# Optimization experiments

Hardware: AMD Instinct MI355X
Metric: run time of the kernel (lower is better)

Reference implementation:

```python
import jax, jax.numpy as jnp
import numpy as np

EPS_BN = 1e-5


def _square_distance(a, b):
    # a: [B,N,3], b: [B,S,3] -> [B,N,S]
    return (jnp.sum(a * a, -1)[:, :, None]
            - 2.0 * jnp.einsum('bnc,bsc->bns', a, b)
            + jnp.sum(b * b, -1)[:, None, :])


def _bn_relu(x, gamma, beta):
    # x: [B,C,N]; training-mode batch norm over (B,N) per channel
    mean = jnp.mean(x, axis=(0, 2), keepdims=True)
    var = jnp.var(x, axis=(0, 2), keepdims=True)
    y = (x - mean) * jax.lax.rsqrt(var + EPS_BN)
    y = y * gamma[None, :, None] + beta[None, :, None]
    return jax.nn.relu(y)


def setup_inputs() -> dict:
    key = jax.random.key(0)
    ks = jax.random.split(key, 8)
    B, N, S, D1, D2 = 16, 4096, 1024, 128, 256
    Cin, C0, C1 = D1 + D2, 256, 128
    inp = {
        'xyz1': jax.random.normal(ks[0], (B, 3, N), jnp.float32),
        'xyz2': jax.random.normal(ks[1], (B, 3, S), jnp.float32),
        'points1': jax.random.normal(ks[2], (B, D1, N), jnp.float32),
        'points2': jax.random.normal(ks[3], (B, D2, S), jnp.float32),
        # pointwise Conv1d weights (kernel size 1) as [out,in]
        'w0': jax.random.normal(ks[4], (C0, Cin), jnp.float32) * (1.0 / np.sqrt(Cin)),
        'b0': jnp.zeros((C0,), jnp.float32),
        'g0': jnp.ones((C0,), jnp.float32),
        'be0': jnp.zeros((C0,), jnp.float32),
        'w1': jax.random.normal(ks[5], (C1, C0), jnp.float32) * (1.0 / np.sqrt(C0)),
        'b1': jnp.zeros((C1,), jnp.float32),
        'g1': jnp.ones((C1,), jnp.float32),
        'be1': jnp.zeros((C1,), jnp.float32),
    }
    return inp


def reference(xyz1, xyz2, points1, points2, w0, b0, g0, be0, w1, b1, g1, be1):
    # permute to [B,N,3] / [B,S,3] / [B,S,D2]
    x1 = jnp.transpose(xyz1, (0, 2, 1))
    x2 = jnp.transpose(xyz2, (0, 2, 1))
    p2 = jnp.transpose(points2, (0, 2, 1))
    B, N, _ = x1.shape

    dists = _square_distance(x1, x2)            # [B,N,S]
    # NOTE: faithful to the source: idx comes from the sort, but the
    # weight distances are the FIRST 3 columns of the UNsorted dists
    # (the repo assigns sorted values to `dicts`, not `dists`).
    idx = jnp.argsort(dists, axis=-1)[:, :, :3]  # [B,N,3]
    d3 = jnp.maximum(dists[:, :, :3], 1e-10)     # [B,N,3]
    weight = 1.0 / d3
    weight = weight / jnp.sum(weight, axis=-1, keepdims=True)

    gathered = jax.vmap(lambda p, i: p[i])(p2, idx)          # [B,N,3,D2]
    interpolated = jnp.sum(gathered * weight[..., None], axis=2)  # [B,N,D2]

    p1 = jnp.transpose(points1, (0, 2, 1))       # [B,N,D1]
    new_points = jnp.concatenate([p1, interpolated], axis=-1)  # [B,N,Cin]
    new_points = jnp.transpose(new_points, (0, 2, 1))           # [B,Cin,N]

    h = jnp.einsum('oc,bcn->bon', w0, new_points) + b0[None, :, None]
    h = _bn_relu(h, g0, be0)
    h = jnp.einsum('oc,bcn->bon', w1, h) + b1[None, :, None]
    h = _bn_relu(h, g1, be1)
    return h
```

## Files before the change

### kernel.cpp

```cpp
#include <hip/hip_runtime.h>
#include <cstdint>
#include <cstddef>

#define BB   16
#define NN   4096
#define SS   1024
#define D1   128
#define D2   256
#define CIN  384
#define C0   256
#define C1   128
#define MM   (BB*NN)
#define NBLK (MM/128)

typedef __attribute__((ext_vector_type(8))) short short8;
typedef __attribute__((ext_vector_type(4))) float f32x4;

__device__ __forceinline__ float b2f(unsigned short h) {
    union { unsigned int u; float f; } x; x.u = ((unsigned int)h) << 16; return x.f;
}
__device__ __forceinline__ unsigned short f2b(float f) {
    union { float f; unsigned int u; } x; x.f = f;
    unsigned int r = x.u + 0x7FFFu + ((x.u >> 16) & 1u);
    return (unsigned short)(r >> 16);
}

#define GLD16(g, l) __builtin_amdgcn_global_load_lds( \
    (const __attribute__((address_space(1))) void*)(g), \
    (__attribute__((address_space(3))) void*)(l), 16, 0, 0)

__device__ __forceinline__ void knn_body5(const float* __restrict__ xyz1,
                                          const float* __restrict__ xyz2,
                                          int* __restrict__ idxb, float* __restrict__ wtb,
                                          int rb, int t, char* smem)
{
    float4* cnd = (float4*)smem;
    const int b    = rb >> 7;
    const int bx   = rb & 127;
    const int chunk = t & 7;
    const int n    = bx * 32 + (t >> 3);

    for (int i = t; i < SS; i += 256) {
        float qx = xyz2[((size_t)b * 3 + 0) * SS + i];
        float qy = xyz2[((size_t)b * 3 + 1) * SS + i];
        float qz = xyz2[((size_t)b * 3 + 2) * SS + i];
        cnd[(i >> 7) * 129 + (i & 127)] = make_float4(qx, qy, qz, 0.f);
    }
    __syncthreads();

    const float px = xyz1[((size_t)b * 3 + 0) * NN + n];
    const float py = xyz1[((size_t)b * 3 + 1) * NN + n];
    const float pz = xyz1[((size_t)b * 3 + 2) * NN + n];

    const double INITK = __hiloint2double(0x7F7FFFFF, 0);
    double A0 = INITK, A1 = INITK, A2 = INITK;
    double B0 = INITK, B1 = INITK, B2 = INITK;
    const float4* cc = cnd + chunk * 129;
    const int sbase = chunk * 128;

#pragma unroll 4
    for (int c = 0; c < 128; c += 2) {
        {
            float4 q = cc[c];
            float dx = px - q.x, dy = py - q.y, dz = pz - q.z;
            float d = dx*dx + dy*dy + dz*dz;
            double k = __hiloint2double(__float_as_int(d), sbase + c);
            double t0 = fmin(k, A0), h0 = fmax(k, A0);
            double t1 = fmin(h0, A1), h1 = fmax(h0, A1);
            A2 = fmin(h1, A2); A0 = t0; A1 = t1;
        }
        {
            float4 q = cc[c + 1];
            float dx = px - q.x, dy = py - q.y, dz = pz - q.z;
            float d = dx*dx + dy*dy + dz*dz;
            double k = __hiloint2double(__float_as_int(d), sbase + c + 1);
            double t0 = fmin(k, B0), h0 = fmax(k, B0);
            double t1 = fmin(h0, B1), h1 = fmax(h0, B1);
            B2 = fmin(h1, B2); B0 = t0; B1 = t1;
        }
    }

    double K0, K1, K2;
    {
        double y0 = fmax(A0, B0);
        K0 = fmin(A0, B0);
        double x1 = fmin(A1, B1);
        K1 = fmin(y0, x1);
        double z  = fmax(y0, x1);
        K2 = fmin(z, fmin(A2, B2));
    }
#pragma unroll
    for (int r = 1; r <= 4; r <<= 1) {
        double C0d = __shfl_xor(K0, r);
        double C1d = __shfl_xor(K1, r);
        double C2d = __shfl_xor(K2, r);
        double y0 = fmax(K0, C0d);
        K0 = fmin(K0, C0d);
        double x1 = fmin(K1, C1d);
        double nK1 = fmin(y0, x1);
        double z  = fmax(y0, x1);
        K2 = fmin(z, fmin(K2, C2d));
        K1 = nK1;
    }

    if (chunk == 0) {
        int j0 = __double2loint(K0), j1 = __double2loint(K1), j2 = __double2loint(K2);
        float4 q0 = cnd[0], q1 = cnd[1], q2 = cnd[2];
        float dd0, dd1, dd2;
        { float dx=px-q0.x, dy=py-q0.y, dz=pz-q0.z; dd0 = fmaxf(dx*dx+dy*dy+dz*dz, 1e-10f); }
        { float dx=px-q1.x, dy=py-q1.y, dz=pz-q1.z; dd1 = fmaxf(dx*dx+dy*dy+dz*dz, 1e-10f); }
        { float dx=px-q2.x, dy=py-q2.y, dz=pz-q2.z; dd2 = fmaxf(dx*dx+dy*dy+dz*dz, 1e-10f); }
        float r0 = 1.f/dd0, r1 = 1.f/dd1, r2 = 1.f/dd2;
        float inv = 1.f / (r0 + r1 + r2);
        size_t base = ((size_t)b * NN + n) * 3;
        idxb[base+0] = j0; idxb[base+1] = j1; idxb[base+2] = j2;
        wtb[base+0] = r0*inv; wtb[base+1] = r1*inv; wtb[base+2] = r2*inv;
    }
}

__device__ __forceinline__ void transpose_body(const float* __restrict__ src,
                                               unsigned short* __restrict__ dst,
                                               int C, int Np, int dstStride,
                                               int b, int cblk, int nblk, int t, char* smem)
{
    float (*tile)[65] = (float(*)[65])smem;
    const int c0 = cblk * 64, n0 = nblk * 64;
    const int j = t & 63, i4 = t >> 6;
#pragma unroll
    for (int p = 0; p < 64; p += 4) {
        int ci = p + i4;
        tile[ci][j] = src[((size_t)b * C + c0 + ci) * Np + n0 + j];
    }
    __syncthreads();
#pragma unroll
    for (int p = 0; p < 64; p += 4) {
        int ni = p + i4;
        dst[((size_t)b * Np + n0 + ni) * dstStride + c0 + j] = f2b(tile[j][ni]);
    }
}

__global__ __launch_bounds__(256) void mega_front_k(
    const float* __restrict__ xyz1, const float* __restrict__ xyz2,
    const float* __restrict__ points1, const float* __restrict__ points2,
    const float* __restrict__ w0, const float* __restrict__ w1,
    unsigned short* __restrict__ P1T, unsigned short* __restrict__ P2T,
    unsigned short* __restrict__ w0b, unsigned short* __restrict__ w1b,
    int* __restrict__ idxb, float* __restrict__ wtb)
{
    __shared__ __align__(16) char smem[16640];
    const unsigned bid = blockIdx.x;
    const int g = bid / 86, r = bid % 86;
    const int t = threadIdx.x;

    if (r < 32) {
        knn_body5(xyz1, xyz2, idxb, wtb, g * 32 + r, t, smem);
    } else if (r < 64) {
        int rb = g * 32 + (r - 32);
        transpose_body(points1, P1T, D1, NN, D1,
                       rb >> 7, (rb >> 6) & 1, rb & 63, t, smem);
    } else if (r < 80) {
        int rb = g * 16 + (r - 64);
        transpose_body(points2, P2T, D2, SS, D2,
                       rb >> 6, (rb >> 4) & 3, rb & 15, t, smem);
    } else {
        int rb = g * 6 + (r - 80);
        int i = rb * 256 + t;
        if (i < C0 * CIN) w0b[i] = f2b(w0[i]);
        if (i < C1 * C0)  w1b[i] = f2b(w1[i]);
    }
}

__launch_bounds__(512, 1)
__global__ void gemm1_k(const unsigned short* __restrict__ P1T,
                        const unsigned short* __restrict__ P2T,
                        const int* __restrict__ idxb, const float* __restrict__ wtb,
                        const unsigned short* __restrict__ w0b,
                        unsigned short* __restrict__ h1, float* __restrict__ part1)
{
    __shared__ unsigned short Als[128 * 64];
    __shared__ unsigned short Bls[256 * 64];
    __shared__ float lsum[2][256];
    __shared__ float lsq[2][256];

    const int t = threadIdx.x;
    const int wv = t >> 6, l = t & 63, g = l >> 4, lc = l & 15;
    const int wm = wv >> 2, wn = wv & 3;
    const int m0 = blockIdx.x * 128;
    const int b  = blockIdx.x >> 5;
    const int sub = t & 7;

    const int grow = t >> 2;
    const size_t gb = ((size_t)(m0 + grow)) * 3;
    const int gi0 = idxb[gb], gi1 = idxb[gb+1], gi2 = idxb[gb+2];
    const float gw0 = wtb[gb], gw1 = wtb[gb+1], gw2 = wtb[gb+2];
    const char* gp0 = (const char*)(P2T + ((size_t)b * SS + gi0) * D2) + (t & 3) * 32;
    const char* gp1 = (const char*)(P2T + ((size_t)b * SS + gi1) * D2) + (t & 3) * 32;
    const char* gp2 = (const char*)(P2T + ((size_t)b * SS + gi2) * D2) + (t & 3) * 32;
    char* gdst = (char*)Als + grow * 128;
    const int gsw = (grow & 7) << 4;

    f32x4 acc[4][4];
#pragma unroll
    for (int i = 0; i < 4; ++i)
#pragma unroll
        for (int j = 0; j < 4; ++j) acc[i][j] = (f32x4){0.f, 0.f, 0.f, 0.f};

    for (int ks = 0; ks < 6; ++ks) {
        const int k0 = ks * 64;
        __syncthreads();
        if (ks < 2) {
#pragma unroll
            for (int q = 0; q < 2; ++q) {
                int row = q * 64 + (t >> 3);
                int bco = (sub * 16) ^ ((row & 7) << 4);
                const char* src = (const char*)P1T + (((size_t)(m0 + row)) * D1 + k0) * 2 + bco;
                char* dst = (char*)Als + (q * 512 + wv * 64) * 16;
                GLD16(src, dst);
            }
        } else {
            const int cgB = (ks - 2) * 128;
#pragma unroll
            for (int h = 0; h < 2; ++h) {
                union { uint4 v; unsigned short s[8]; } a0, a1, a2, ov;
                a0.v = *(const uint4*)(gp0 + cgB + h * 16);
                a1.v = *(const uint4*)(gp1 + cgB + h * 16);
                a2.v = *(const uint4*)(gp2 + cgB + h * 16);
#pragma unroll
                for (int i = 0; i < 8; ++i)
                    ov.s[i] = f2b(gw0 * b2f(a0.s[i]) + gw1 * b2f(a1.s[i]) + gw2 * b2f(a2.s[i]));
                *(uint4*)(gdst + (((t & 3) * 32 + h * 16) ^ gsw)) = ov.v;
            }
        }
#pragma unroll
        for (int q = 0; q < 4; ++q) {
            int o = q * 64 + (t >> 3);
            int bco = (sub * 16) ^ ((o & 7) << 4);
            const char* src = (const char*)w0b + (((size_t)o) * CIN + k0) * 2 + bco;
            char* dst = (char*)Bls + (q * 512 + wv * 64) * 16;
            GLD16(src, dst);
        }
        __syncthreads();
#pragma unroll
        for (int kk = 0; kk < 2; ++kk) {
            short8 af[4], bfr[4];
#pragma unroll
            for (int fm = 0; fm < 4; ++fm) {
                int row = wm * 64 + fm * 16 + lc;
                int bcol = kk * 64 + g * 16;
                af[fm] = *(const short8*)((const char*)Als + row * 128 + (bcol ^ ((row & 7) << 4)));
            }
#pragma unroll
            for (int fn = 0; fn < 4; ++fn) {
                int o = wn * 64 + fn * 16 + lc;
                int bcol = kk * 64 + g * 16;
                bfr[fn] = *(const short8*)((const char*)Bls + o * 128 + (bcol ^ ((o & 7) << 4)));
            }
#pragma unroll
            for (int fm = 0; fm < 4; ++fm)
#pragma unroll
                for (int fn = 0; fn < 4; ++fn)
                    acc[fm][fn] = __builtin_amdgcn_mfma_f32_16x16x32_bf16(af[fm], bfr[fn], acc[fm][fn], 0, 0, 0);
        }
    }

    float s1[4] = {0,0,0,0}, s2v[4] = {0,0,0,0};
#pragma unroll
    for (int fm = 0; fm < 4; ++fm)
#pragma unroll
        for (int fn = 0; fn < 4; ++fn) {
            int row = m0 + wm * 64 + fm * 16 + g * 4;
            int col = wn * 64 + fn * 16 + lc;
#pragma unroll
            for (int j = 0; j < 4; ++j) {
                float v = acc[fm][fn][j];
                h1[((size_t)(row + j)) * C0 + col] = f2b(v);
                s1[fn] += v; s2v[fn] += v * v;
            }
        }
#pragma unroll
    for (int fn = 0; fn < 4; ++fn) {
        s1[fn] += __shfl_xor(s1[fn], 16); s1[fn] += __shfl_xor(s1[fn], 32);
        s2v[fn] += __shfl_xor(s2v[fn], 16); s2v[fn] += __shfl_xor(s2v[fn], 32);
    }
    if (l < 16) {
#pragma unroll
        for (int fn = 0; fn < 4; ++fn) {
            lsum[wm][wn * 64 + fn * 16 + l] = s1[fn];
            lsq[wm][wn * 64 + fn * 16 + l] = s2v[fn];
        }
    }
    __syncthreads();
    if (t < 256) {
        part1[(size_t)t * NBLK + blockIdx.x]        = lsum[0][t] + lsum[1][t];
        part1[(size_t)(C0 + t) * NBLK + blockIdx.x] = lsq[0][t] + lsq[1][t];
    }
}

__global__ void stats_k(const float* __restrict__ part, int nblk, int C,
                        const float* __restrict__ gam, const float* __restrict__ bet,
                        float* __restrict__ sc, float* __restrict__ sh)
{
    const int w = threadIdx.x >> 6, l = threadIdx.x & 63;
    const int o = blockIdx.x * 4 + w;
    if (o >= C) return;
    float s = 0.f, q = 0.f;
    for (int i = l; i < nblk; i += 64) {
        s += part[(size_t)o * nblk + i];
        q += part[(size_t)(C + o) * nblk + i];
    }
#pragma unroll
    for (int r = 32; r; r >>= 1) { s += __shfl_xor(s, r); q += __shfl_xor(q, r); }
    if (l == 0) {
        const float inv = 1.0f / (float)MM;
        float mean = s * inv;
        float var = q * inv - mean * mean;
        float scale = gam[o] * rsqrtf(var + 1e-5f);
        sc[o] = scale;
        sh[o] = bet[o] - mean * scale;
    }
}

__launch_bounds__(256, 1)
__global__ void gemm2_k(const unsigned short* __restrict__ h1, const unsigned short* __restrict__ w1b,
                        const float* __restrict__ sc1, const float* __restrict__ sh1,
                        unsigned short* __restrict__ h2, float* __restrict__ part2)
{
    __shared__ unsigned short Als[128 * 64];
    __shared__ unsigned short Bls[128 * 64];
    __shared__ float scl[256], shl[256];
    __shared__ float lsum[2][128];
    __shared__ float lsq[2][128];

    const int t = threadIdx.x;
    const int wv = t >> 6, l = t & 63, g = l >> 4, lc = l & 15;
    const int wm = wv >> 1, wn = wv & 1;
    const int m0 = blockIdx.x * 128;
    const int sub = t & 7;

    scl[t] = sc1[t]; shl[t] = sh1[t];

    f32x4 acc[4][4];
#pragma unroll
    for (int i = 0; i < 4; ++i)
#pragma unroll
        for (int j = 0; j < 4; ++j) acc[i][j] = (f32x4){0.f, 0.f, 0.f, 0.f};

    for (int ks = 0; ks < 4; ++ks) {
        const int k0 = ks * 64;
        __syncthreads();
        uint4 r[4];
#pragma unroll
        for (int q = 0; q < 4; ++q) {
            int row = q * 32 + (t >> 3);
            r[q] = *(const uint4*)((const char*)h1 + (((size_t)(m0 + row)) * C0 + k0) * 2 + sub * 16);
        }
#pragma unroll
        for (int q = 0; q < 4; ++q) {
            int row = q * 32 + (t >> 3);
            union { uint4 v; unsigned short s[8]; } u, ov;
            u.v = r[q];
#pragma unroll
            for (int i = 0; i < 8; ++i) {
                int k = k0 + sub * 8 + i;
                float f = b2f(u.s[i]);
                ov.s[i] = f2b(fmaxf(0.0f, fmaf(scl[k], f, shl[k])));
            }
            *(uint4*)((char*)Als + row * 128 + ((sub * 16) ^ ((row & 7) << 4))) = ov.v;
        }
#pragma unroll
        for (int q = 0; q < 4; ++q) {
            int o = q * 32 + (t >> 3);
            int bco = (sub * 16) ^ ((o & 7) << 4);
            const char* src = (const char*)w1b + (((size_t)o) * C0 + k0) * 2 + bco;
            char* dst = (char*)Bls + (q * 256 + wv * 64) * 16;
            GLD16(src, dst);
        }
        __syncthreads();
#pragma unroll
        for (int kk = 0; kk < 2; ++kk) {
            short8 af[4], bfr[4];
#pragma unroll
            for (int fm = 0; fm < 4; ++fm) {
                int row = wm * 64 + fm * 16 + lc;
                int bcol = kk * 64 + g * 16;
                af[fm] = *(const short8*)((const char*)Als + row * 128 + (bcol ^ ((row & 7) << 4)));
            }
#pragma unroll
            for (int fn = 0; fn < 4; ++fn) {
                int o = wn * 64 + fn * 16 + lc;
                int bcol = kk * 64 + g * 16;
                bfr[fn] = *(const short8*)((const char*)Bls + o * 128 + (bcol ^ ((o & 7) << 4)));
            }
#pragma unroll
            for (int fm = 0; fm < 4; ++fm)
#pragma unroll
                for (int fn = 0; fn < 4; ++fn)
                    acc[fm][fn] = __builtin_amdgcn_mfma_f32_16x16x32_bf16(af[fm], bfr[fn], acc[fm][fn], 0, 0, 0);
        }
    }

    float s1[4] = {0,0,0,0}, s2v[4] = {0,0,0,0};
#pragma unroll
    for (int fm = 0; fm < 4; ++fm)
#pragma unroll
        for (int fn = 0; fn < 4; ++fn) {
            int row = m0 + wm * 64 + fm * 16 + g * 4;
            int col = wn * 64 + fn * 16 + lc;
#pragma unroll
            for (int j = 0; j < 4; ++j) {
                float v = acc[fm][fn][j];
                h2[((size_t)(row + j)) * C1 + col] = f2b(v);
                s1[fn] += v; s2v[fn] += v * v;
            }
        }
#pragma unroll
    for (int fn = 0; fn < 4; ++fn) {
        s1[fn] += __shfl_xor(s1[fn], 16); s1[fn] += __shfl_xor(s1[fn], 32);
        s2v[fn] += __shfl_xor(s2v[fn], 16); s2v[fn] += __shfl_xor(s2v[fn], 32);
    }
    if (l < 16) {
#pragma unroll
        for (int fn = 0; fn < 4; ++fn) {
            lsum[wm][wn * 64 + fn * 16 + l] = s1[fn];
            lsq[wm][wn * 64 + fn * 16 + l] = s2v[fn];
        }
    }
    __syncthreads();
    if (t < 128) {
        part2[(size_t)t * NBLK + blockIdx.x]        = lsum[0][t] + lsum[1][t];
        part2[(size_t)(C1 + t) * NBLK + blockIdx.x] = lsq[0][t] + lsq[1][t];
    }
}

__global__ void finalize_k(const unsigned short* __restrict__ h2,
                           const float* __restrict__ sc, const float* __restrict__ sh,
                           float* __restrict__ out)
{
    __shared__ float tile[64][65];
    const int b = blockIdx.z, o0 = blockIdx.y * 64, n0 = blockIdx.x * 64;
    const int t = threadIdx.x, j = t & 63, i4 = t >> 6;
    const float scv = sc[o0 + j], shv = sh[o0 + j];
#pragma unroll
    for (int p = 0; p < 64; p += 4) {
        int ni = p + i4;
        float f = b2f(h2[((size_t)b * NN + n0 + ni) * C1 + o0 + j]);
        tile[ni][j] = fmaxf(0.0f, fmaf(scv, f, shv));
    }
    __syncthreads();
#pragma unroll
    for (int p = 0; p < 64; p += 4) {
        int oi = p + i4;
        out[((size_t)(b * C1 + o0 + oi)) * NN + n0 + j] = tile[j][oi];
    }
}

extern "C" void kernel_launch(void* const* d_in, const int* in_sizes, int n_in,
                              void* d_out, int out_size, void* d_ws, size_t ws_size,
                              hipStream_t stream)
{
    const float* xyz1    = (const float*)d_in[0];
    const float* xyz2    = (const float*)d_in[1];
    const float* points1 = (const float*)d_in[2];
    const float* points2 = (const float*)d_in[3];
    const float* w0      = (const float*)d_in[4];
    const float* g0      = (const float*)d_in[6];
    const float* be0     = (const float*)d_in[7];
    const float* w1      = (const float*)d_in[8];
    const float* g1      = (const float*)d_in[10];
    const float* be1     = (const float*)d_in[11];
    float* out = (float*)d_out;
    char* ws = (char*)d_ws;

    unsigned short* P1T = (unsigned short*)(ws + 0);
    unsigned short* h1  = (unsigned short*)(ws + 16777216);
    unsigned short* P2T = (unsigned short*)(ws + 50331648);
    unsigned short* h2  = (unsigned short*)(ws + 58720256);
    int*   idxb  = (int*)  (ws + 75497472);
    float* wtb   = (float*)(ws + 76283904);
    unsigned short* w0b = (unsigned short*)(ws + 77070336);
    unsigned short* w1b = (unsigned short*)(ws + 77266944);
    float* part1 = (float*)(ws + 77332480);
    float* part2 = (float*)(ws + 78381056);
    float* sc1   = (float*)(ws + 78905344);
    float* sh1   = (float*)(ws + 78906368);
    float* sc2   = (float*)(ws + 78907392);
    float* sh2   = (float*)(ws + 78908416);

    mega_front_k<<<86 * 64, 256, 0, stream>>>(xyz1, xyz2, points1, points2, w0, w1,
                                              P1T, P2T, w0b, w1b, idxb, wtb);
    gemm1_k<<<MM/128, 512, 0, stream>>>(P1T, P2T, idxb, wtb, w0b, h1, part1);
    stats_k<<<C0/4, 256, 0, stream>>>(part1, NBLK, C0, g0, be0, sc1, sh1);
    gemm2_k<<<MM/128, 256, 0, stream>>>(h1, w1b, sc1, sh1, h2, part2);
    stats_k<<<C1/4, 256, 0, stream>>>(part2, NBLK, C1, g1, be1, sc2, sh2);
    finalize_k<<<dim3(NN/64, C1/64, BB), 256, 0, stream>>>(h2, sc2, sh2, out);
}
```

Measured before the change: 113.9 us.

## Split KNN search over two candidate halves and merge top-3 in gemm1

The KNN search is split so each block scans only half of the 1024 candidates, which doubles the KNN block count and shortens each block's serial loop. Each half writes its packed (distance, index) top-3 as doubles to a workspace buffer. gemm1 reads both halves and merges them into the final top-3 before the gather. Launch-bound occupancy hints for both GEMMs also change from 1 to 4 blocks per CU. The cost is extra global traffic for the partial triples and a few extra merge ops in gemm1.

```diff
diff --git a/kernel.cpp b/kernel.cpp
--- a/kernel.cpp
+++ b/kernel.cpp
@@ -29,22 +29,25 @@
     (const __attribute__((address_space(1))) void*)(g), \
     (__attribute__((address_space(3))) void*)(l), 16, 0, 0)
 
-__device__ __forceinline__ void knn_body5(const float* __restrict__ xyz1,
+__device__ __forceinline__ void knn_body7(const float* __restrict__ xyz1,
                                           const float* __restrict__ xyz2,
-                                          int* __restrict__ idxb, float* __restrict__ wtb,
-                                          int rb, int t, char* smem)
+                                          double* __restrict__ trip, float* __restrict__ wtb,
+                                          int kb, int t, char* smem)
 {
     float4* cnd = (float4*)smem;
-    const int b    = rb >> 7;
-    const int bx   = rb & 127;
+    const int h    = kb & 1;
+    const int pb   = kb >> 1;
+    const int b    = pb >> 7;
+    const int bx   = pb & 127;
     const int chunk = t & 7;
     const int n    = bx * 32 + (t >> 3);
 
-    for (int i = t; i < SS; i += 256) {
-        float qx = xyz2[((size_t)b * 3 + 0) * SS + i];
-        float qy = xyz2[((size_t)b * 3 + 1) * SS + i];
-        float qz = xyz2[((size_t)b * 3 + 2) * SS + i];
-        cnd[(i >> 7) * 129 + (i & 127)] = make_float4(qx, qy, qz, 0.f);
+    for (int i = t; i < 512; i += 256) {
+        int s = h * 512 + i;
+        float qx = xyz2[((size_t)b * 3 + 0) * SS + s];
+        float qy = xyz2[((size_t)b * 3 + 1) * SS + s];
+        float qz = xyz2[((size_t)b * 3 + 2) * SS + s];
+        cnd[(i >> 6) * 65 + (i & 63)] = make_float4(qx, qy, qz, 0.f);
     }
     __syncthreads();
 
@@ -55,11 +58,11 @@
     const double INITK = __hiloint2double(0x7F7FFFFF, 0);
     double A0 = INITK, A1 = INITK, A2 = INITK;
     double B0 = INITK, B1 = INITK, B2 = INITK;
-    const float4* cc = cnd + chunk * 129;
-    const int sbase = chunk * 128;
+    const float4* cc = cnd + chunk * 65;
+    const int sbase = h * 512 + chunk * 64;
 
 #pragma unroll 4
-    for (int c = 0; c < 128; c += 2) {
+    for (int c = 0; c < 64; c += 2) {
         {
             float4 q = cc[c];
             float dx = px - q.x, dy = py - q.y, dz = pz - q.z;
@@ -104,17 +107,19 @@
     }
 
     if (chunk == 0) {
-        int j0 = __double2loint(K0), j1 = __double2loint(K1), j2 = __double2loint(K2);
-        float4 q0 = cnd[0], q1 = cnd[1], q2 = cnd[2];
-        float dd0, dd1, dd2;
-        { float dx=px-q0.x, dy=py-q0.y, dz=pz-q0.z; dd0 = fmaxf(dx*dx+dy*dy+dz*dz, 1e-10f); }
-        { float dx=px-q1.x, dy=py-q1.y, dz=pz-q1.z; dd1 = fmaxf(dx*dx+dy*dy+dz*dz, 1e-10f); }
-        { float dx=px-q2.x, dy=py-q2.y, dz=pz-q2.z; dd2 = fmaxf(dx*dx+dy*dy+dz*dz, 1e-10f); }
-        float r0 = 1.f/dd0, r1 = 1.f/dd1, r2 = 1.f/dd2;
-        float inv = 1.f / (r0 + r1 + r2);
-        size_t base = ((size_t)b * NN + n) * 3;
-        idxb[base+0] = j0; idxb[base+1] = j1; idxb[base+2] = j2;
-        wtb[base+0] = r0*inv; wtb[base+1] = r1*inv; wtb[base+2] = r2*inv;
+        size_t m = (size_t)b * NN + n;
+        double* tp = trip + ((size_t)h * MM + m) * 3;
+        tp[0] = K0; tp[1] = K1; tp[2] = K2;
+        if (h == 0) {
+            float4 q0 = cnd[0], q1 = cnd[1], q2 = cnd[2];
+            float dd0, dd1, dd2;
+            { float dx=px-q0.x, dy=py-q0.y, dz=pz-q0.z; dd0 = fmaxf(dx*dx+dy*dy+dz*dz, 1e-10f); }
+            { float dx=px-q1.x, dy=py-q1.y, dz=pz-q1.z; dd1 = fmaxf(dx*dx+dy*dy+dz*dz, 1e-10f); }
+            { float dx=px-q2.x, dy=py-q2.y, dz=pz-q2.z; dd2 = fmaxf(dx*dx+dy*dy+dz*dz, 1e-10f); }
+            float r0 = 1.f/dd0, r1 = 1.f/dd1, r2 = 1.f/dd2;
+            float inv = 1.f / (r0 + r1 + r2);
+            wtb[m*3+0] = r0*inv; wtb[m*3+1] = r1*inv; wtb[m*3+2] = r2*inv;
+        }
     }
 }
 
@@ -145,35 +150,35 @@
     const float* __restrict__ w0, const float* __restrict__ w1,
     unsigned short* __restrict__ P1T, unsigned short* __restrict__ P2T,
     unsigned short* __restrict__ w0b, unsigned short* __restrict__ w1b,
-    int* __restrict__ idxb, float* __restrict__ wtb)
+    double* __restrict__ trip, float* __restrict__ wtb)
 {
     __shared__ __align__(16) char smem[16640];
     const unsigned bid = blockIdx.x;
-    const int g = bid / 86, r = bid % 86;
+    const int g = bid / 118, r = bid % 118;
     const int t = threadIdx.x;
 
-    if (r < 32) {
-        knn_body5(xyz1, xyz2, idxb, wtb, g * 32 + r, t, smem);
-    } else if (r < 64) {
-        int rb = g * 32 + (r - 32);
+    if (r < 64) {
+        knn_body7(xyz1, xyz2, trip, wtb, g * 64 + r, t, smem);
+    } else if (r < 96) {
+        int rb = g * 32 + (r - 64);
         transpose_body(points1, P1T, D1, NN, D1,
                        rb >> 7, (rb >> 6) & 1, rb & 63, t, smem);
-    } else if (r < 80) {
-        int rb = g * 16 + (r - 64);
+    } else if (r < 112) {
+        int rb = g * 16 + (r - 96);
         transpose_body(points2, P2T, D2, SS, D2,
                        rb >> 6, (rb >> 4) & 3, rb & 15, t, smem);
     } else {
-        int rb = g * 6 + (r - 80);
+        int rb = g * 6 + (r - 112);
         int i = rb * 256 + t;
         if (i < C0 * CIN) w0b[i] = f2b(w0[i]);
         if (i < C1 * C0)  w1b[i] = f2b(w1[i]);
     }
 }
 
-__launch_bounds__(512, 1)
+__launch_bounds__(512, 4)
 __global__ void gemm1_k(const unsigned short* __restrict__ P1T,
                         const unsigned short* __restrict__ P2T,
-                        const int* __restrict__ idxb, const float* __restrict__ wtb,
+                        const double* __restrict__ trip, const float* __restrict__ wtb,
                         const unsigned short* __restrict__ w0b,
                         unsigned short* __restrict__ h1, float* __restrict__ part1)
 {
@@ -190,9 +195,18 @@
     const int sub = t & 7;
 
     const int grow = t >> 2;
-    const size_t gb = ((size_t)(m0 + grow)) * 3;
-    const int gi0 = idxb[gb], gi1 = idxb[gb+1], gi2 = idxb[gb+2];
-    const float gw0 = wtb[gb], gw1 = wtb[gb+1], gw2 = wtb[gb+2];
+    const size_t gm = (size_t)(m0 + grow);
+    const double* tpA = trip + gm * 3;
+    const double* tpB = trip + ((size_t)MM + gm) * 3;
+    double hA0 = tpA[0], hA1 = tpA[1], hA2 = tpA[2];
+    double hB0 = tpB[0], hB1 = tpB[1], hB2 = tpB[2];
+    double y0 = fmax(hA0, hB0), K0 = fmin(hA0, hB0);
+    double x1 = fmin(hA1, hB1), K1 = fmin(y0, x1);
+    double z  = fmax(y0, x1),   K2 = fmin(z, fmin(hA2, hB2));
+    const int gi0 = __double2loint(K0);
+    const int gi1 = __double2loint(K1);
+    const int gi2 = __double2loint(K2);
+    const float gw0 = wtb[gm*3], gw1 = wtb[gm*3+1], gw2 = wtb[gm*3+2];
     const char* gp0 = (const char*)(P2T + ((size_t)b * SS + gi0) * D2) + (t & 3) * 32;
     const char* gp1 = (const char*)(P2T + ((size_t)b * SS + gi1) * D2) + (t & 3) * 32;
     const char* gp2 = (const char*)(P2T + ((size_t)b * SS + gi2) * D2) + (t & 3) * 32;
@@ -320,7 +334,7 @@
     }
 }
 
-__launch_bounds__(256, 1)
+__launch_bounds__(256, 4)
 __global__ void gemm2_k(const unsigned short* __restrict__ h1, const unsigned short* __restrict__ w1b,
                         const float* __restrict__ sc1, const float* __restrict__ sh1,
                         unsigned short* __restrict__ h2, float* __restrict__ part2)
@@ -475,20 +489,20 @@
     unsigned short* h1  = (unsigned short*)(ws + 16777216);
     unsigned short* P2T = (unsigned short*)(ws + 50331648);
     unsigned short* h2  = (unsigned short*)(ws + 58720256);
-    int*   idxb  = (int*)  (ws + 75497472);
-    float* wtb   = (float*)(ws + 76283904);
-    unsigned short* w0b = (unsigned short*)(ws + 77070336);
-    unsigned short* w1b = (unsigned short*)(ws + 77266944);
-    float* part1 = (float*)(ws + 77332480);
-    float* part2 = (float*)(ws + 78381056);
-    float* sc1   = (float*)(ws + 78905344);
-    float* sh1   = (float*)(ws + 78906368);
-    float* sc2   = (float*)(ws + 78907392);
-    float* sh2   = (float*)(ws + 78908416);
-
-    mega_front_k<<<86 * 64, 256, 0, stream>>>(xyz1, xyz2, points1, points2, w0, w1,
-                                              P1T, P2T, w0b, w1b, idxb, wtb);
-    gemm1_k<<<MM/128, 512, 0, stream>>>(P1T, P2T, idxb, wtb, w0b, h1, part1);
+    double* trip = (double*)(ws + 75497472);
+    float* wtb   = (float*)(ws + 78643200);
+    unsigned short* w0b = (unsigned short*)(ws + 79429632);
+    unsigned short* w1b = (unsigned short*)(ws + 79626240);
+    float* part1 = (float*)(ws + 79691776);
+    float* part2 = (float*)(ws + 80740352);
+    float* sc1   = (float*)(ws + 81264640);
+    float* sh1   = (float*)(ws + 81265664);
+    float* sc2   = (float*)(ws + 81266688);
+    float* sh2   = (float*)(ws + 81267712);
+
+    mega_front_k<<<118 * 64, 256, 0, stream>>>(xyz1, xyz2, points1, points2, w0, w1,
+                                               P1T, P2T, w0b, w1b, trip, wtb);
+    gemm1_k<<<MM/128, 512, 0, stream>>>(P1T, P2T, trip, wtb, w0b, h1, part1);
     stats_k<<<C0/4, 256, 0, stream>>>(part1, NBLK, C0, g0, be0, sc1, sh1);
     gemm2_k<<<MM/128, 256, 0, stream>>>(h1, w1b, sc1, sh1, h2, part2);
     stats_k<<<C1/4, 256, 0, stream>>>(part2, NBLK, C1, g1, be1, sc2, sh2);
```

New measurement: 108.6 us. 1.05x faster.
